# Kernel tuning notes

Hardware: AMD Instinct MI355X
Metric: run time of the kernel (lower is better)

The kernel has to match this reference:

```python
import jax, jax.numpy as jnp
import numpy as np

STRIDE = 1
PADDING = 1


def setup_inputs() -> dict:
    key = jax.random.key(0)
    k1, k2 = jax.random.split(key)
    x = jax.random.normal(k1, (32, 64, 112, 112), dtype=jnp.float32)
    weights = jax.random.normal(k2, (128, 64, 3, 3), dtype=jnp.float32)
    biases = jnp.zeros((128,), dtype=jnp.float32)
    return {"x": x, "weights": weights, "biases": biases}


def reference(x, weights, biases):
    # NCHW input, OIHW weights -> NCHW output; zero padding, stride 1.
    out = jax.lax.conv_general_dilated(
        x, weights,
        window_strides=(STRIDE, STRIDE),
        padding=((PADDING, PADDING), (PADDING, PADDING)),
        dimension_numbers=("NCHW", "OIHW", "NCHW"),
    )
    return out + biases[None, :, None, None]
```

## Files before the change

### kernel.cpp

```cpp
#include <hip/hip_runtime.h>
#include <stdint.h>

typedef unsigned short u16;
typedef __attribute__((ext_vector_type(8))) short bf16x8;
typedef __attribute__((ext_vector_type(4))) float f32x4;

#define C_IN    64
#define K_OUT   128
#define HW      112
#define HW2     (HW * HW)
#define CP      72
#define NW      114
#define THREADS 256

__device__ __forceinline__ u16 f2bf(float f) {
  union { float f; uint32_t u; } x; x.f = f;
  return (u16)((x.u + 0x7FFFu + ((x.u >> 16) & 1u)) >> 16);
}

__global__ void prep_weights(const float* __restrict__ w, u16* __restrict__ wt) {
  int idx = blockIdx.x * 256 + threadIdx.x;
  if (idx >= K_OUT * C_IN * 9) return;
  int c    = idx & (C_IN - 1);
  int kout = (idx >> 6) & (K_OUT - 1);
  int rs   = idx >> 13;
  wt[idx] = f2bf(w[(kout * C_IN + c) * 9 + rs]);
}

__global__ __launch_bounds__(THREADS, 2) void conv3x3(
    const float* __restrict__ x, const u16* __restrict__ wt,
    const float* __restrict__ bias, float* __restrict__ out) {
  __shared__ u16 Xs[3][NW][CP];
  __shared__ u16 Ws[K_OUT][CP];

  const int tid = threadIdx.x;
  const int bid = blockIdx.x;
  const int n = bid / HW;
  const int h = bid % HW;

  {
    uint32_t* p = (uint32_t*)&Xs[0][0][0];
    const int tot = 3 * NW * CP / 2;
    for (int i = tid; i < tot; i += THREADS) p[i] = 0u;
  }
  __syncthreads();

  const float* xn = x + (size_t)n * C_IN * HW2;
  for (int r = 0; r < 3; ++r) {
    int row = h + r - 1;
    if (row < 0 || row >= HW) continue;
    const float* xrow = xn + (size_t)row * HW;
    for (int t = tid; t < 32 * 28; t += THREADS) {
      int w4 = t % 28;
      int cp = t / 28;
      int c  = cp * 2;
      float4 va = *(const float4*)(xrow + (size_t)c * HW2 + w4 * 4);
      float4 vb = *(const float4*)(xrow + (size_t)(c + 1) * HW2 + w4 * 4);
      int wb = 1 + w4 * 4;
      *(uint32_t*)&Xs[r][wb + 0][c] = (uint32_t)f2bf(va.x) | ((uint32_t)f2bf(vb.x) << 16);
      *(uint32_t*)&Xs[r][wb + 1][c] = (uint32_t)f2bf(va.y) | ((uint32_t)f2bf(vb.y) << 16);
      *(uint32_t*)&Xs[r][wb + 2][c] = (uint32_t)f2bf(va.z) | ((uint32_t)f2bf(vb.z) << 16);
      *(uint32_t*)&Xs[r][wb + 3][c] = (uint32_t)f2bf(va.w) | ((uint32_t)f2bf(vb.w) << 16);
    }
  }

  const int lane = tid & 63;
  const int wave = tid >> 6;
  const int quad = lane >> 4;
  const int l15  = lane & 15;
  const int kb   = wave * 32;

  f32x4 acc[2][7];
#pragma unroll
  for (int i = 0; i < 2; ++i)
#pragma unroll
    for (int j = 0; j < 7; ++j) acc[i][j] = (f32x4){0.f, 0.f, 0.f, 0.f};

  for (int rs = 0; rs < 9; ++rs) {
    const int r = rs / 3;
    const int s = rs % 3;

    __syncthreads();
    {
      const u16* wsrc = wt + rs * (K_OUT * C_IN);
#pragma unroll
      for (int t8 = 0; t8 < (K_OUT * C_IN / 8) / THREADS; ++t8) {
        int t = tid + t8 * THREADS;
        int kout = t >> 3;
        int cc = (t & 7) * 8;
        *(uint4*)&Ws[kout][cc] = *(const uint4*)(wsrc + t * 8);
      }
    }
    __syncthreads();

#pragma unroll
    for (int ch = 0; ch < 2; ++ch) {
      const int c0 = ch * 32 + quad * 8;
      bf16x8 a0 = *(const bf16x8*)&Ws[kb + l15][c0];
      bf16x8 a1 = *(const bf16x8*)&Ws[kb + 16 + l15][c0];
#pragma unroll
      for (int wt7 = 0; wt7 < 7; ++wt7) {
        bf16x8 b = *(const bf16x8*)&Xs[r][wt7 * 16 + l15 + s][c0];
        acc[0][wt7] = __builtin_amdgcn_mfma_f32_16x16x32_bf16(a0, b, acc[0][wt7], 0, 0, 0);
        acc[1][wt7] = __builtin_amdgcn_mfma_f32_16x16x32_bf16(a1, b, acc[1][wt7], 0, 0, 0);
      }
    }
  }

  float* on = out + (size_t)n * K_OUT * HW2 + (size_t)h * HW;
#pragma unroll
  for (int mt = 0; mt < 2; ++mt) {
#pragma unroll
    for (int rg = 0; rg < 4; ++rg) {
      const int kout = kb + mt * 16 + quad * 4 + rg;
      const float bv = bias[kout];
      float* orow = on + (size_t)kout * HW2;
#pragma unroll
      for (int wt7 = 0; wt7 < 7; ++wt7) {
        orow[wt7 * 16 + l15] = acc[mt][wt7][rg] + bv;
      }
    }
  }
}

extern "C" void kernel_launch(void* const* d_in, const int* in_sizes, int n_in,
                              void* d_out, int out_size, void* d_ws, size_t ws_size,
                              hipStream_t stream) {
  const float* x  = (const float*)d_in[0];
  const float* w  = (const float*)d_in[1];
  const float* bi = (const float*)d_in[2];
  float* out = (float*)d_out;
  u16* wt = (u16*)d_ws;

  prep_weights<<<(K_OUT * C_IN * 9 + 255) / 256, 256, 0, stream>>>(w, wt);
  conv3x3<<<32 * HW, THREADS, 0, stream>>>(x, wt, bi, out);
}
```

Before: 365.1 us.

## Load weight fragments directly from global memory, drop LDS weight staging and syncs

Removes the shared-memory weight tile and its per-tap load plus two barriers. MFMA A-operands now come straight from global/L2. It also zeroes only the halo columns and boundary rows instead of the whole input tile, merges the three row loads into one flat loop with channel-fastest indexing, and swizzles block IDs across 8 groups. Dropping the weight tile cuts LDS use, so occupancy is raised to 3 blocks per CU, at the cost of relying on cache hits for repeated weight reads.

```diff
diff --git a/kernel.cpp b/kernel.cpp
--- a/kernel.cpp
+++ b/kernel.cpp
@@ -27,42 +27,57 @@
   wt[idx] = f2bf(w[(kout * C_IN + c) * 9 + rs]);
 }
 
-__global__ __launch_bounds__(THREADS, 2) void conv3x3(
+__global__ __launch_bounds__(THREADS, 3) void conv3x3(
     const float* __restrict__ x, const u16* __restrict__ wt,
     const float* __restrict__ bias, float* __restrict__ out) {
   __shared__ u16 Xs[3][NW][CP];
-  __shared__ u16 Ws[K_OUT][CP];
 
   const int tid = threadIdx.x;
+
   const int bid = blockIdx.x;
-  const int n = bid / HW;
-  const int h = bid % HW;
+  const int lb  = (bid & 7) * 448 + (bid >> 3);
+  const int n = lb / HW;
+  const int h = lb % HW;
 
-  {
-    uint32_t* p = (uint32_t*)&Xs[0][0][0];
-    const int tot = 3 * NW * CP / 2;
-    for (int i = tid; i < tot; i += THREADS) p[i] = 0u;
+  if (tid < 192) {
+    const int seg  = tid >> 5;
+    const int cd   = (tid & 31) * 2;
+    const int r    = seg >> 1;
+    const int wcol = (seg & 1) ? (NW - 1) : 0;
+    *(uint32_t*)&Xs[r][wcol][cd] = 0u;
   }
-  __syncthreads();
+  if (h == 0) {
+    for (int t = tid; t < NW * 32; t += THREADS)
+      *(uint32_t*)&Xs[0][t >> 5][(t & 31) * 2] = 0u;
+  } else if (h == HW - 1) {
+    for (int t = tid; t < NW * 32; t += THREADS)
+      *(uint32_t*)&Xs[2][t >> 5][(t & 31) * 2] = 0u;
+  }
 
   const float* xn = x + (size_t)n * C_IN * HW2;
-  for (int r = 0; r < 3; ++r) {
-    int row = h + r - 1;
-    if (row < 0 || row >= HW) continue;
-    const float* xrow = xn + (size_t)row * HW;
-    for (int t = tid; t < 32 * 28; t += THREADS) {
-      int w4 = t % 28;
-      int cp = t / 28;
-      int c  = cp * 2;
-      float4 va = *(const float4*)(xrow + (size_t)c * HW2 + w4 * 4);
-      float4 vb = *(const float4*)(xrow + (size_t)(c + 1) * HW2 + w4 * 4);
-      int wb = 1 + w4 * 4;
-      *(uint32_t*)&Xs[r][wb + 0][c] = (uint32_t)f2bf(va.x) | ((uint32_t)f2bf(vb.x) << 16);
-      *(uint32_t*)&Xs[r][wb + 1][c] = (uint32_t)f2bf(va.y) | ((uint32_t)f2bf(vb.y) << 16);
-      *(uint32_t*)&Xs[r][wb + 2][c] = (uint32_t)f2bf(va.z) | ((uint32_t)f2bf(vb.z) << 16);
-      *(uint32_t*)&Xs[r][wb + 3][c] = (uint32_t)f2bf(va.w) | ((uint32_t)f2bf(vb.w) << 16);
+  for (int it = 0; it < 11; ++it) {
+    const int task = tid + it * THREADS;
+    if (task < 3 * 28 * 32) {
+      const int cp   = task & 31;
+      const int rest = task >> 5;
+      const int w4   = rest % 28;
+      const int r    = rest / 28;
+      const int row  = h + r - 1;
+      if (row >= 0 && row < HW) {
+        const float* xrow = xn + (size_t)(2 * cp) * HW2 + (size_t)row * HW + w4 * 4;
+        const float4 va = *(const float4*)(xrow);
+        const float4 vb = *(const float4*)(xrow + HW2);
+        const int wb = 1 + w4 * 4;
+        const int c  = 2 * cp;
+        *(uint32_t*)&Xs[r][wb + 0][c] = (uint32_t)f2bf(va.x) | ((uint32_t)f2bf(vb.x) << 16);
+        *(uint32_t*)&Xs[r][wb + 1][c] = (uint32_t)f2bf(va.y) | ((uint32_t)f2bf(vb.y) << 16);
+        *(uint32_t*)&Xs[r][wb + 2][c] = (uint32_t)f2bf(va.z) | ((uint32_t)f2bf(vb.z) << 16);
+        *(uint32_t*)&Xs[r][wb + 3][c] = (uint32_t)f2bf(va.w) | ((uint32_t)f2bf(vb.w) << 16);
+      }
     }
   }
+
+  __syncthreads();
 
   const int lane = tid & 63;
   const int wave = tid >> 6;
@@ -76,33 +91,21 @@
 #pragma unroll
     for (int j = 0; j < 7; ++j) acc[i][j] = (f32x4){0.f, 0.f, 0.f, 0.f};
 
+#pragma unroll
   for (int rs = 0; rs < 9; ++rs) {
     const int r = rs / 3;
     const int s = rs % 3;
-
-    __syncthreads();
-    {
-      const u16* wsrc = wt + rs * (K_OUT * C_IN);
-#pragma unroll
-      for (int t8 = 0; t8 < (K_OUT * C_IN / 8) / THREADS; ++t8) {
-        int t = tid + t8 * THREADS;
-        int kout = t >> 3;
-        int cc = (t & 7) * 8;
-        *(uint4*)&Ws[kout][cc] = *(const uint4*)(wsrc + t * 8);
-      }
-    }
-    __syncthreads();
-
+    const u16* wbase = wt + rs * (K_OUT * C_IN);
 #pragma unroll
     for (int ch = 0; ch < 2; ++ch) {
       const int c0 = ch * 32 + quad * 8;
-      bf16x8 a0 = *(const bf16x8*)&Ws[kb + l15][c0];
-      bf16x8 a1 = *(const bf16x8*)&Ws[kb + 16 + l15][c0];
+      const bf16x8 a0 = *(const bf16x8*)(wbase + (kb + l15) * C_IN + c0);
+      const bf16x8 a1 = *(const bf16x8*)(wbase + (kb + 16 + l15) * C_IN + c0);
 #pragma unroll
-      for (int wt7 = 0; wt7 < 7; ++wt7) {
-        bf16x8 b = *(const bf16x8*)&Xs[r][wt7 * 16 + l15 + s][c0];
-        acc[0][wt7] = __builtin_amdgcn_mfma_f32_16x16x32_bf16(a0, b, acc[0][wt7], 0, 0, 0);
-        acc[1][wt7] = __builtin_amdgcn_mfma_f32_16x16x32_bf16(a1, b, acc[1][wt7], 0, 0, 0);
+      for (int w7 = 0; w7 < 7; ++w7) {
+        const bf16x8 b = *(const bf16x8*)&Xs[r][w7 * 16 + l15 + s][c0];
+        acc[0][w7] = __builtin_amdgcn_mfma_f32_16x16x32_bf16(a0, b, acc[0][w7], 0, 0, 0);
+        acc[1][w7] = __builtin_amdgcn_mfma_f32_16x16x32_bf16(a1, b, acc[1][w7], 0, 0, 0);
       }
     }
   }
@@ -116,8 +119,8 @@
       const float bv = bias[kout];
       float* orow = on + (size_t)kout * HW2;
 #pragma unroll
-      for (int wt7 = 0; wt7 < 7; ++wt7) {
-        orow[wt7 * 16 + l15] = acc[mt][wt7][rg] + bv;
+      for (int w7 = 0; w7 < 7; ++w7) {
+        orow[w7 * 16 + l15] = acc[mt][w7][rg] + bv;
       }
     }
   }
```

After: 378.4 us. +3.6%, slower.
